# Optimization experiments

Measured on AMD Instinct MI355X. Metric: run time of the kernel, lower is better.

Reference implementation:

```python
import jax, jax.numpy as jnp
import numpy as np

B, S, D = 4, 2048, 1024
E, K, H = 8, 2, 4096


def setup_inputs() -> dict:
    key = jax.random.key(0)
    ks = jax.random.split(key, 8)
    sd = 1.0 / np.sqrt(D)
    sh = 1.0 / np.sqrt(H)
    x = jax.random.normal(ks[0], (B, S, D), dtype=jnp.float32)
    gate_w = jax.random.normal(ks[1], (D, E), dtype=jnp.float32) * sd
    gate_b = jnp.zeros((E,), dtype=jnp.float32)
    w1 = jax.random.normal(ks[2], (E, D, H), dtype=jnp.float32) * sd
    b1 = jnp.zeros((E, H), dtype=jnp.float32)
    w2 = jax.random.normal(ks[3], (E, H, D), dtype=jnp.float32) * sh
    b2 = jnp.zeros((E, D), dtype=jnp.float32)
    return {"x": x, "gate_w": gate_w, "gate_b": gate_b,
            "w1": w1, "b1": b1, "w2": w2, "b2": b2}


def reference(x, gate_w, gate_b, w1, b1, w2, b2):
    # gate logits [B,S,E]
    logits = jnp.einsum('bsd,de->bse', x, gate_w) + gate_b
    # top-k over experts, softmax over the k selected (dim=2), in float32
    weights, selected = jax.lax.top_k(logits, K)            # [B,S,K]
    weights = jax.nn.softmax(weights.astype(jnp.float32), axis=-1).astype(x.dtype)
    out = jnp.zeros_like(x)
    for i in range(E):
        # per-token combine weight for expert i (0 if not routed here)
        w_i = jnp.sum(jnp.where(selected == i, weights, 0.0), axis=-1)  # [B,S]
        h = jax.nn.gelu(jnp.einsum('bsd,dh->bsh', x, w1[i]) + b1[i])    # [B,S,H]
        y = jnp.einsum('bsh,hd->bsd', h, w2[i]) + b2[i]                  # [B,S,D]
        out = out + w_i[..., None] * y
    return out
```

## Files before the change

### kernel.cpp

```cpp
#include <hip/hip_runtime.h>
#include <hip/hip_bf16.h>
#include <stdint.h>

#define T_TOK 8192
#define D_DIM 1024
#define E_NUM 8
#define H_DIM 4096
#define NPAD 144
#define PPX (NPAD / 8)

typedef short bf16x8 __attribute__((ext_vector_type(8)));
typedef float f32x4 __attribute__((ext_vector_type(4)));
typedef unsigned short usv8 __attribute__((ext_vector_type(8)));

#define AS1 __attribute__((address_space(1)))
#define AS3 __attribute__((address_space(3)))

__device__ __forceinline__ unsigned short f2b(float f) {
  union { float f; uint32_t u; } v; v.f = f;
  uint32_t r = (v.u + 0x7fffu + ((v.u >> 16) & 1u)) >> 16;
  return (unsigned short)r;
}

__device__ __forceinline__ float gelu_tanh(float x) {
  float u = 0.7978845608028654f * (x + 0.044715f * x * x * x);
  u = fminf(fmaxf(u, -15.f), 15.f);
  float e = __expf(2.f * u);
  float t = (e - 1.f) / (e + 1.f);
  return 0.5f * x * (1.f + t);
}

__device__ __forceinline__ void gload_lds16(const void* g, void* l) {
  __builtin_amdgcn_global_load_lds((const AS1 uint32_t*)g, (AS3 uint32_t*)l, 16, 0, 0);
}

__global__ __launch_bounds__(256) void moe_gate_conv(const float* __restrict__ x,
                                                     const float* __restrict__ gw,
                                                     const float* __restrict__ gb,
                                                     unsigned short* __restrict__ xb,
                                                     int2* __restrict__ sel,
                                                     float2* __restrict__ wts,
                                                     int* __restrict__ meta) {
  int lane = threadIdx.x & 63;
  int t = blockIdx.x * 4 + (threadIdx.x >> 6);
  const float* xr = x + (size_t)t * D_DIM;
  unsigned short* xo = xb + (size_t)t * D_DIM;
  float acc[8];
#pragma unroll
  for (int e = 0; e < 8; e++) acc[e] = 0.f;
#pragma unroll
  for (int i = 0; i < 4; i++) {
    int d0 = lane * 4 + i * 256;
    float4 xv = *(const float4*)(xr + d0);
    ushort4 o;
    o.x = f2b(xv.x); o.y = f2b(xv.y); o.z = f2b(xv.z); o.w = f2b(xv.w);
    *(ushort4*)(xo + d0) = o;
    const float* gp = gw + (size_t)d0 * 8;
    float xs[4] = {xv.x, xv.y, xv.z, xv.w};
#pragma unroll
    for (int j = 0; j < 4; j++) {
#pragma unroll
      for (int e = 0; e < 8; e++) acc[e] += xs[j] * gp[j * 8 + e];
    }
  }
#pragma unroll
  for (int off = 32; off > 0; off >>= 1) {
#pragma unroll
    for (int e = 0; e < 8; e++) acc[e] += __shfl_xor(acc[e], off);
  }
  if (lane == 0) {
    float lg[8];
#pragma unroll
    for (int e = 0; e < 8; e++) lg[e] = acc[e] + gb[e];
    int e0 = 0; float b0 = lg[0];
#pragma unroll
    for (int e = 1; e < 8; e++) if (lg[e] > b0) { b0 = lg[e]; e0 = e; }
    int e1 = -1; float b1v = -1e30f;
#pragma unroll
    for (int e = 0; e < 8; e++) if (e != e0 && lg[e] > b1v) { b1v = lg[e]; e1 = e; }
    float d = __expf(b1v - b0);
    float w0 = 1.f / (1.f + d), w1 = d / (1.f + d);
    sel[t] = make_int2(e0, e1);
    wts[t] = make_float2(w0, w1);
    atomicAdd(&meta[e0], 1);
    atomicAdd(&meta[e1], 1);
  }
}

__global__ __launch_bounds__(256) void moe_transpose2(const float* __restrict__ w1,
                                                      const float* __restrict__ w2,
                                                      unsigned short* __restrict__ w1t,
                                                      unsigned short* __restrict__ w2t) {
  int z = blockIdx.y;
  int e = z & 7;
  const float* in; unsigned short* out; int R, C, cy, ry;
  if (z < 8) { in = w1 + (size_t)e * D_DIM * H_DIM; out = w1t + (size_t)e * D_DIM * H_DIM;
               R = D_DIM; C = H_DIM; cy = blockIdx.x & 63; ry = blockIdx.x >> 6; }
  else       { in = w2 + (size_t)e * H_DIM * D_DIM; out = w2t + (size_t)e * H_DIM * D_DIM;
               R = H_DIM; C = D_DIM; cy = blockIdx.x & 15; ry = blockIdx.x >> 4; }
  int r0 = ry * 64, c0 = cy * 64;
  __shared__ float tile[64][65];
  int t = threadIdx.x;
  int ir = t >> 4, ic = (t & 15) * 4;
#pragma unroll
  for (int p = 0; p < 4; ++p) {
    float4 v = *(const float4*)(in + (size_t)(r0 + ir + p * 16) * C + c0 + ic);
    tile[ir + p * 16][ic] = v.x;     tile[ir + p * 16][ic + 1] = v.y;
    tile[ir + p * 16][ic + 2] = v.z; tile[ir + p * 16][ic + 3] = v.w;
  }
  __syncthreads();
  int orow = t >> 3, oc = (t & 7) * 8;
#pragma unroll
  for (int q = 0; q < 2; ++q) {
    int r = orow + q * 32;
    usv8 o;
#pragma unroll
    for (int j = 0; j < 8; ++j) o[j] = f2b(tile[oc + j][r]);
    *(usv8*)(out + (size_t)(c0 + r) * R + r0 + oc) = o;
  }
}

__global__ void moe_scan(int* meta, int2* wl) {
  if (threadIdx.x == 0 && blockIdx.x == 0) {
    int o = 0;
    for (int e = 0; e < 8; e++) { meta[8 + e] = o; meta[20 + e] = o; o += meta[e]; }
    meta[16] = o;
    int w = 0;
    for (int e = 0; e < 8; e++)
      for (int m0 = 0; m0 < meta[e]; m0 += 128) wl[w++] = make_int2(e, m0);
    meta[17] = w;
  }
}

__global__ __launch_bounds__(256) void moe_scatter(const int2* __restrict__ sel,
                                                   const float2* __restrict__ wts,
                                                   int* __restrict__ meta,
                                                   int* __restrict__ token_id,
                                                   float* __restrict__ weightv) {
  int t = blockIdx.x * 256 + threadIdx.x;
  if (t >= T_TOK) return;
  int2 s = sel[t];
  float2 w = wts[t];
  int p0 = atomicAdd(&meta[20 + s.x], 1); token_id[p0] = t; weightv[p0] = w.x;
  int p1 = atomicAdd(&meta[20 + s.y], 1); token_id[p1] = t; weightv[p1] = w.y;
}

__global__ __launch_bounds__(256) void moe_outinit(const int2* __restrict__ sel,
                                                   const float2* __restrict__ wts,
                                                   const float* __restrict__ b2,
                                                   float* __restrict__ out) {
  int t = blockIdx.x;
  int d = threadIdx.x * 4;
  int2 s = sel[t];
  float2 w = wts[t];
  float4 a = *(const float4*)(b2 + (size_t)s.x * D_DIM + d);
  float4 b = *(const float4*)(b2 + (size_t)s.y * D_DIM + d);
  float4 o;
  o.x = w.x * a.x + w.y * b.x;
  o.y = w.x * a.y + w.y * b.y;
  o.z = w.x * a.z + w.y * b.z;
  o.w = w.x * a.w + w.y * b.w;
  *(float4*)(out + (size_t)t * D_DIM + d) = o;
}

__global__ __launch_bounds__(256, 4) void moe_gemm1(const unsigned short* __restrict__ xb,
                                                    const unsigned short* __restrict__ w1t,
                                                    const float* __restrict__ b1,
                                                    const int* __restrict__ meta,
                                                    const int2* __restrict__ wl,
                                                    const int* __restrict__ token_id,
                                                    unsigned short* __restrict__ hbuf) {
  int b = blockIdx.x;
  int c = b & 7, u = b >> 3;
  int n = u & 31, ps = u >> 5;
  int wi = c * PPX + ps;
  if (wi >= meta[17]) return;
  int e = wl[wi].x, m0 = wl[wi].y;
  int seg = meta[8 + e], ne = meta[9 + e] - seg;
  int n0 = n * 128;
  const unsigned short* wB = w1t + (size_t)e * H_DIM * D_DIM;

  __shared__ unsigned short As[2][4096];
  __shared__ unsigned short Bs[2][4096];

  int tid = threadIdx.x, lane = tid & 63, wv = tid >> 6;
  const unsigned short* aptr[2];
  const unsigned short* bptr[2];
#pragma unroll
  for (int q = 0; q < 2; q++) {
    int chunk = tid + q * 256;
    int row = chunk >> 2;
    int ko = (chunk & 3) * 8;
    int gi = m0 + row; if (gi >= ne) gi = m0;
    int tok = token_id[seg + gi];
    aptr[q] = xb + (size_t)tok * D_DIM + ko;
    bptr[q] = wB + (size_t)(n0 + row) * D_DIM + ko;
  }
  auto stage = [&](int buf, int kt) {
#pragma unroll
    for (int q = 0; q < 2; q++) {
      gload_lds16(aptr[q] + kt * 32, &As[buf][(wv + 4 * q) * 512]);
      gload_lds16(bptr[q] + kt * 32, &Bs[buf][(wv + 4 * q) * 512]);
    }
  };

  f32x4 acc[4][4] = {};
  int wr = wv >> 1, wc = wv & 1;
  int abase = (wr * 64 + (lane & 15)) * 32 + (lane >> 4) * 8;
  int bbase = (wc * 64 + (lane & 15)) * 32 + (lane >> 4) * 8;

  stage(0, 0);
  __syncthreads();
  const int nk = D_DIM / 32;
  for (int kt = 0; kt < nk; ++kt) {
    int cur = kt & 1;
    if (kt + 1 < nk) stage(cur ^ 1, kt + 1);
    bf16x8 af[4], bfr[4];
#pragma unroll
    for (int m = 0; m < 4; m++) af[m] = *(const bf16x8*)&As[cur][abase + m * 512];
#pragma unroll
    for (int nn = 0; nn < 4; nn++) bfr[nn] = *(const bf16x8*)&Bs[cur][bbase + nn * 512];
#pragma unroll
    for (int m = 0; m < 4; m++)
#pragma unroll
      for (int nn = 0; nn < 4; nn++)
        acc[m][nn] = __builtin_amdgcn_mfma_f32_16x16x32_bf16(af[m], bfr[nn], acc[m][nn], 0, 0, 0);
    __syncthreads();
  }

  int rbase = wr * 64 + (lane >> 4) * 4;
  int cbase = n0 + wc * 64 + (lane & 15);
  const float* b1e = b1 + (size_t)e * H_DIM + cbase;
  float bv[4];
#pragma unroll
  for (int nn = 0; nn < 4; nn++) bv[nn] = b1e[nn * 16];
#pragma unroll
  for (int m = 0; m < 4; m++) {
#pragma unroll
    for (int j = 0; j < 4; j++) {
      int gi = m0 + rbase + m * 16 + j;
      if (gi < ne) {
        unsigned short* hrow = hbuf + (size_t)(seg + gi) * H_DIM + cbase;
#pragma unroll
        for (int nn = 0; nn < 4; nn++) {
          float v = acc[m][nn][j] + bv[nn];
          hrow[nn * 16] = f2b(gelu_tanh(v));
        }
      }
    }
  }
}

__global__ __launch_bounds__(256, 4) void moe_gemm2(const unsigned short* __restrict__ hbuf,
                                                    const unsigned short* __restrict__ w2t,
                                                    const int* __restrict__ meta,
                                                    const int2* __restrict__ wl,
                                                    const int* __restrict__ token_id,
                                                    const float* __restrict__ weightv,
                                                    float* __restrict__ out) {
  int b = blockIdx.x;
  int c = b & 7, u = b >> 3;
  int n = u & 7, ks = (u >> 3) & 1, ps = u >> 4;
  int wi = c * PPX + ps;
  if (wi >= meta[17]) return;
  int e = wl[wi].x, m0 = wl[wi].y;
  int seg = meta[8 + e], ne = meta[9 + e] - seg;
  int n0 = n * 128;
  int kbase = ks * 2048;
  const unsigned short* wB = w2t + (size_t)e * D_DIM * H_DIM;

  __shared__ unsigned short As[2][4096];
  __shared__ unsigned short Bs[2][4096];

  int tid = threadIdx.x, lane = tid & 63, wv = tid >> 6;
  const unsigned short* aptr[2];
  const unsigned short* bptr[2];
#pragma unroll
  for (int q = 0; q < 2; q++) {
    int chunk = tid + q * 256;
    int row = chunk >> 2;
    int ko = (chunk & 3) * 8;
    int gi = m0 + row; if (gi >= ne) gi = m0;
    aptr[q] = hbuf + (size_t)(seg + gi) * H_DIM + kbase + ko;
    bptr[q] = wB + (size_t)(n0 + row) * H_DIM + kbase + ko;
  }
  auto stage = [&](int buf, int kt) {
#pragma unroll
    for (int q = 0; q < 2; q++) {
      gload_lds16(aptr[q] + kt * 32, &As[buf][(wv + 4 * q) * 512]);
      gload_lds16(bptr[q] + kt * 32, &Bs[buf][(wv + 4 * q) * 512]);
    }
  };

  f32x4 acc[4][4] = {};
  int wr = wv >> 1, wc = wv & 1;
  int abase = (wr * 64 + (lane & 15)) * 32 + (lane >> 4) * 8;
  int bbase = (wc * 64 + (lane & 15)) * 32 + (lane >> 4) * 8;

  stage(0, 0);
  __syncthreads();
  const int nk = 2048 / 32;
  for (int kt = 0; kt < nk; ++kt) {
    int cur = kt & 1;
    if (kt + 1 < nk) stage(cur ^ 1, kt + 1);
    bf16x8 af[4], bfr[4];
#pragma unroll
    for (int m = 0; m < 4; m++) af[m] = *(const bf16x8*)&As[cur][abase + m * 512];
#pragma unroll
    for (int nn = 0; nn < 4; nn++) bfr[nn] = *(const bf16x8*)&Bs[cur][bbase + nn * 512];
#pragma unroll
    for (int m = 0; m < 4; m++)
#pragma unroll
      for (int nn = 0; nn < 4; nn++)
        acc[m][nn] = __builtin_amdgcn_mfma_f32_16x16x32_bf16(af[m], bfr[nn], acc[m][nn], 0, 0, 0);
    __syncthreads();
  }

  int rbase = wr * 64 + (lane >> 4) * 4;
  int cbase = n0 + wc * 64 + (lane & 15);
#pragma unroll
  for (int m = 0; m < 4; m++) {
#pragma unroll
    for (int j = 0; j < 4; j++) {
      int gi = m0 + rbase + m * 16 + j;
      if (gi < ne) {
        int p = seg + gi;
        int tok = token_id[p];
        float wt = weightv[p];
        float* orow = out + (size_t)tok * D_DIM + cbase;
#pragma unroll
        for (int nn = 0; nn < 4; nn++)
          atomicAdd(&orow[nn * 16], wt * acc[m][nn][j]);
      }
    }
  }
}

extern "C" void kernel_launch(void* const* d_in, const int* in_sizes, int n_in,
                              void* d_out, int out_size, void* d_ws, size_t ws_size,
                              hipStream_t stream) {
  const float* x      = (const float*)d_in[0];
  const float* gate_w = (const float*)d_in[1];
  const float* gate_b = (const float*)d_in[2];
  const float* w1     = (const float*)d_in[3];
  const float* b1     = (const float*)d_in[4];
  const float* w2     = (const float*)d_in[5];
  const float* b2     = (const float*)d_in[6];
  float* out = (float*)d_out;

  uint8_t* ws = (uint8_t*)d_ws;
  unsigned short* hbuf = (unsigned short*)(ws);
  unsigned short* xb   = (unsigned short*)(ws + 134217728ull);
  unsigned short* w1t  = (unsigned short*)(ws + 150994944ull);
  unsigned short* w2t  = (unsigned short*)(ws + 218103808ull);
  int*    token_id = (int*)  (ws + 285212672ull);
  float*  weightv  = (float*)(ws + 285278208ull);
  float2* wts      = (float2*)(ws + 285343744ull);
  int2*   sel      = (int2*) (ws + 285409280ull);
  int*    meta     = (int*)  (ws + 285474816ull);
  int2*   wl       = (int2*) (ws + 285475328ull);

  hipMemsetAsync(meta, 0, 512, stream);

  moe_gate_conv<<<dim3(T_TOK / 4), 256, 0, stream>>>(x, gate_w, gate_b, xb, sel, wts, meta);
  moe_transpose2<<<dim3(1024, 16), 256, 0, stream>>>(w1, w2, w1t, w2t);
  moe_scan<<<1, 64, 0, stream>>>(meta, wl);
  moe_scatter<<<dim3(T_TOK / 256), 256, 0, stream>>>(sel, wts, meta, token_id, weightv);
  moe_outinit<<<dim3(T_TOK), 256, 0, stream>>>(sel, wts, b2, out);

  moe_gemm1<<<dim3(NPAD * 32), 256, 0, stream>>>(xb, w1t, b1, meta, wl, token_id, hbuf);
  moe_gemm2<<<dim3(NPAD * 16), 256, 0, stream>>>(hbuf, w2t, meta, wl, token_id, weightv, out);
}
```

Before: 852.1 us.

## Triple-buffer gemm1 LDS pipeline with a single barrier and parallelize moe_scan

Moves the first expert GEMM from a double-buffered LDS loop with two syncthreads per k-step to a three-stage ring. Each step waits on vmcnt, issues one barrier, then prefetches two tiles ahead, so global-to-LDS loads overlap more MFMA work. LDS use grows to 48KB per block, which may lower occupancy under launch_bounds(256,4). Separately, the serial single-thread scan that built the work list is replaced by a parallel one where each of 256 threads computes its own entry.

```diff
diff --git a/kernel.cpp b/kernel.cpp
--- a/kernel.cpp
+++ b/kernel.cpp
@@ -120,16 +120,32 @@
   }
 }
 
-__global__ void moe_scan(int* meta, int2* wl) {
-  if (threadIdx.x == 0 && blockIdx.x == 0) {
+__global__ __launch_bounds__(256) void moe_scan(int* meta, int2* wl) {
+  int cnt[8];
+#pragma unroll
+  for (int e = 0; e < 8; e++) cnt[e] = meta[e];
+  int t = threadIdx.x;
+  if (t < 8) {
     int o = 0;
-    for (int e = 0; e < 8; e++) { meta[8 + e] = o; meta[20 + e] = o; o += meta[e]; }
+    for (int e = 0; e < 8; e++) if (e < t) o += cnt[e];
+    meta[8 + t] = o;
+    meta[20 + t] = o;
+  }
+  if (t == 8) {
+    int o = 0;
+#pragma unroll
+    for (int e = 0; e < 8; e++) o += cnt[e];
     meta[16] = o;
-    int w = 0;
-    for (int e = 0; e < 8; e++)
-      for (int m0 = 0; m0 < meta[e]; m0 += 128) wl[w++] = make_int2(e, m0);
-    meta[17] = w;
-  }
+  }
+  int acc = 0, eSel = -1, base = 0;
+#pragma unroll
+  for (int k = 0; k < 8; k++) {
+    int nxt = acc + ((cnt[k] + 127) >> 7);
+    if (t >= acc && t < nxt) { eSel = k; base = acc; }
+    acc = nxt;
+  }
+  if (t == 9) meta[17] = acc;
+  if (eSel >= 0) wl[t] = make_int2(eSel, (t - base) << 7);
 }
 
 __global__ __launch_bounds__(256) void moe_scatter(const int2* __restrict__ sel,
@@ -180,8 +196,8 @@
   int n0 = n * 128;
   const unsigned short* wB = w1t + (size_t)e * H_DIM * D_DIM;
 
-  __shared__ unsigned short As[2][4096];
-  __shared__ unsigned short Bs[2][4096];
+  __shared__ unsigned short As[3][4096];
+  __shared__ unsigned short Bs[3][4096];
 
   int tid = threadIdx.x, lane = tid & 63, wv = tid >> 6;
   const unsigned short* aptr[2];
@@ -210,11 +226,15 @@
   int bbase = (wc * 64 + (lane & 15)) * 32 + (lane >> 4) * 8;
 
   stage(0, 0);
-  __syncthreads();
+  stage(1, 1);
   const int nk = D_DIM / 32;
+  int cur = 0, sb = 2;
   for (int kt = 0; kt < nk; ++kt) {
-    int cur = kt & 1;
-    if (kt + 1 < nk) stage(cur ^ 1, kt + 1);
+    if (kt < nk - 1) { asm volatile("s_waitcnt vmcnt(4)" ::: "memory"); }
+    else             { asm volatile("s_waitcnt vmcnt(0)" ::: "memory"); }
+    __builtin_amdgcn_s_barrier();
+    __builtin_amdgcn_sched_barrier(0);
+    if (kt + 2 < nk) stage(sb, kt + 2);
     bf16x8 af[4], bfr[4];
 #pragma unroll
     for (int m = 0; m < 4; m++) af[m] = *(const bf16x8*)&As[cur][abase + m * 512];
@@ -225,7 +245,9 @@
 #pragma unroll
       for (int nn = 0; nn < 4; nn++)
         acc[m][nn] = __builtin_amdgcn_mfma_f32_16x16x32_bf16(af[m], bfr[nn], acc[m][nn], 0, 0, 0);
-    __syncthreads();
+    __builtin_amdgcn_sched_barrier(0);
+    cur = (cur == 2) ? 0 : cur + 1;
+    sb  = (sb  == 2) ? 0 : sb  + 1;
   }
 
   int rbase = wr * 64 + (lane >> 4) * 4;
@@ -364,7 +386,7 @@
 
   moe_gate_conv<<<dim3(T_TOK / 4), 256, 0, stream>>>(x, gate_w, gate_b, xb, sel, wts, meta);
   moe_transpose2<<<dim3(1024, 16), 256, 0, stream>>>(w1, w2, w1t, w2t);
-  moe_scan<<<1, 64, 0, stream>>>(meta, wl);
+  moe_scan<<<1, 256, 0, stream>>>(meta, wl);
   moe_scatter<<<dim3(T_TOK / 256), 256, 0, stream>>>(sel, wts, meta, token_id, weightv);
   moe_outinit<<<dim3(T_TOK), 256, 0, stream>>>(sel, wts, b2, out);
 
```

After: 867.4 us. Within noise of the previous version (+1.8%).
